# Kernel optimization log

Hardware: AMD Instinct MI355X
Metric: run time of the kernel (lower is better)

## Reference

```python
import jax, jax.numpy as jnp
import numpy as np

ALPHA = 0.2  # tf.nn.leaky_relu default

def leaky(x):
    return jnp.where(x >= 0, x, ALPHA * x)

def segment_softmax(score, seg, num_segments):
    m = jax.ops.segment_max(score, seg, num_segments=num_segments)
    e = jnp.exp(score - m[seg])
    denom = jax.ops.segment_sum(e, seg, num_segments=num_segments)
    return e / denom[seg]

def setup_inputs() -> dict:
    key = jax.random.key(0)
    ks = jax.random.split(key, 8)
    E, NE, NR, D, U = 500000, 100000, 1000, 128, 128
    return {
        "h_index": jax.random.randint(ks[0], (E,), 0, NE),
        "r_index": jax.random.randint(ks[1], (E,), 0, NR),
        "t_index": jax.random.randint(ks[2], (E,), 0, NE),
        "entity_embeddings": jax.random.normal(ks[3], (NE, D), jnp.float32),
        "relation_embeddings": jax.random.normal(ks[4], (NR, D), jnp.float32),
        "W": jax.random.normal(ks[5], (3 * D, U), jnp.float32) * 0.05,
        "a": jax.random.normal(ks[6], (U, 1), jnp.float32) * 0.1,
        "a_b": jnp.zeros((1,), jnp.float32),
        "bias": jnp.zeros((U,), jnp.float32),
    }

def reference(h_index, r_index, t_index, entity_embeddings, relation_embeddings, W, a, a_b, bias):
    num_entities = entity_embeddings.shape[0]
    h = entity_embeddings[h_index]          # [E, D]
    r = relation_embeddings[r_index]        # [E, D]
    t = entity_embeddings[t_index]          # [E, D]
    feats = jnp.concatenate([h, r, t], axis=-1) @ W  # [E, U]
    # att_kernel Dense(1, activation=leaky_relu), then wrapped again in att_activation
    score = leaky(leaky(feats @ a + a_b))[:, 0]      # [E]
    alpha = segment_softmax(score, h_index, num_entities)
    msg = feats * alpha[:, None]                     # gcn_mapper: edge features * weight
    reduced = jax.ops.segment_sum(msg, h_index, num_segments=num_entities)  # [NE, U]
    out = reduced + bias                             # identity_updater returns reduced_msg
    return jax.nn.relu(out)
```

## Files before the change

### kernel.cpp

```cpp
#include <hip/hip_runtime.h>
#include <hip/hip_bf16.h>

#define ALPHA2 0.04f
#define LDA 136

typedef __attribute__((ext_vector_type(8))) short short8;
typedef __attribute__((ext_vector_type(4))) float floatx4;
typedef __attribute__((ext_vector_type(8))) unsigned short ushort8;

__device__ __forceinline__ unsigned short f2bf(float f) {
    unsigned u = __float_as_uint(f);
    unsigned r = (u + 0x7fffu + ((u >> 16) & 1u)) >> 16;
    return (unsigned short)r;
}
__device__ __forceinline__ float bf2f(unsigned short h) {
    return __uint_as_float((unsigned)h << 16);
}


__global__ void k_prep(const float* __restrict__ W, unsigned short* __restrict__ Bfr,
                       int* __restrict__ count, int NE) {
    int idx = blockIdx.x * blockDim.x + threadIdx.x;
    if (idx < 3 * 128 * 128) {
        int kk = idx & 7, n = (idx >> 3) & 127, g = idx >> 10;
        int slice = g >> 4, kc = (g >> 2) & 3, quad = g & 3;
        int k = kc * 32 + quad * 8 + kk;
        Bfr[idx] = f2bf(W[(size_t)(slice * 128 + k) * 128 + n]);
    }
    if (idx < NE) count[idx] = 0;
}

__global__ __launch_bounds__(256, 4) void k_gemm_all(
        const float* __restrict__ ent, const float* __restrict__ rel,
        const unsigned short* __restrict__ Bfr,
        unsigned short* __restrict__ Pb, unsigned short* __restrict__ Qb,
        unsigned short* __restrict__ Rb,
        float* __restrict__ s1, float* __restrict__ s3, float* __restrict__ s2,
        const float* __restrict__ avec, int NE, int NR, int NBent) {
    __shared__ unsigned short Ash[64 * LDA];
    int tid = threadIdx.x;
    int b = blockIdx.x;
    bool isEnt = b < NBent;
    const float* In = isEnt ? ent : rel;
    int nrows = isEnt ? NE : NR;
    int rowbase = (isEnt ? b : b - NBent) * 64;

    #pragma unroll
    for (int it = 0; it < 8; ++it) {
        int id = it * 256 + tid;
        int chunk = id & 31, row = id >> 5;
        int grow = rowbase + row;
        if (grow > nrows - 1) grow = nrows - 1;
        float4 v = *(const float4*)(In + (size_t)grow * 128 + chunk * 4);
        ushort4 u = make_ushort4(f2bf(v.x), f2bf(v.y), f2bf(v.z), f2bf(v.w));
        *(ushort4*)(Ash + row * LDA + chunk * 4) = u;
    }
    __syncthreads();

    int wave = tid >> 6, lane = tid & 63;
    int m16 = lane & 15, quad = lane >> 4;
    int rs = wave * 16;

    float av[8];
    #pragma unroll
    for (int j = 0; j < 8; ++j) av[j] = avec[j * 16 + m16];

    int nphase = isEnt ? 2 : 1;
    for (int ph = 0; ph < nphase; ++ph) {
        int slice; unsigned short* Out; float* svec;
        if (isEnt) { slice = ph ? 2 : 0; Out = ph ? Qb : Pb; svec = ph ? s3 : s1; }
        else       { slice = 1; Out = Rb; svec = s2; }

        floatx4 acc[8];
        #pragma unroll
        for (int j = 0; j < 8; ++j) acc[j] = (floatx4){0.f, 0.f, 0.f, 0.f};

        short8 bf0[8], bf1[8];
        auto loadB = [&](int kc, short8* dst) {
            const unsigned short* bb =
                Bfr + (size_t)((slice * 4 + kc) * 4 + quad) * 1024 + m16 * 8;
            #pragma unroll
            for (int j = 0; j < 8; ++j) dst[j] = *(const short8*)(bb + j * 128);
        };
        auto doMfma = [&](int kc, short8* bf) {
            short8 af = *(const short8*)(Ash + (rs + m16) * LDA + kc * 32 + quad * 8);
            #pragma unroll
            for (int j = 0; j < 8; ++j)
                acc[j] = __builtin_amdgcn_mfma_f32_16x16x32_bf16(af, bf[j], acc[j], 0, 0, 0);
        };
        loadB(0, bf0);
        loadB(1, bf1);
        doMfma(0, bf0);
        loadB(2, bf0);
        doMfma(1, bf1);
        loadB(3, bf1);
        doMfma(2, bf0);
        doMfma(3, bf1);

        #pragma unroll
        for (int reg = 0; reg < 4; ++reg) {
            int row = rowbase + rs + quad * 4 + reg;
            float part = 0.f;
            ushort8 v;
            #pragma unroll
            for (int j = 0; j < 8; ++j) {
                float x = acc[j][reg];
                part = fmaf(x, av[j], part);
                v[j] = f2bf(x);
            }
            #pragma unroll
            for (int off = 1; off < 16; off <<= 1) part += __shfl_xor(part, off);
            if (row < nrows) {
                *(ushort8*)(Out + (size_t)row * 128 + m16 * 8) = v;
                if (m16 == 0) svec[row] = part;
            }
        }
    }
}

__global__ void k_count(const int* __restrict__ h, int* __restrict__ count,
                        int* __restrict__ rank, int E) {
    int e = blockIdx.x * blockDim.x + threadIdx.x;
    if (e < E) rank[e] = atomicAdd(count + h[e], 1);
}

__device__ __forceinline__ int block_incl_scan256(int s, int* sh, int t) {
    sh[t] = s; __syncthreads();
    #pragma unroll
    for (int off = 1; off < 256; off <<= 1) {
        int x = 0;
        if (t >= off) x = sh[t - off];
        __syncthreads();
        sh[t] += x;
        __syncthreads();
    }
    return sh[t];
}

__global__ __launch_bounds__(256) void k_scan_a(const int* __restrict__ count, int NE,
                                                int* __restrict__ bsum) {
    __shared__ int sh[256];
    int b = blockIdx.x, t = threadIdx.x;
    int base = b * 1024 + t * 4, s = 0;
    #pragma unroll
    for (int j = 0; j < 4; ++j) { int i = base + j; if (i < NE) s += count[i]; }
    sh[t] = s; __syncthreads();
    for (int off = 128; off > 0; off >>= 1) {
        if (t < off) sh[t] += sh[t + off];
        __syncthreads();
    }
    if (t == 0) bsum[b] = sh[0];
}

__global__ __launch_bounds__(256) void k_scan_b(int* __restrict__ bsum, int NB) {
    __shared__ int sh[256];
    int t = threadIdx.x;
    int v[4]; int s = 0;
    #pragma unroll
    for (int j = 0; j < 4; ++j) { int i = t * 4 + j; v[j] = (i < NB) ? bsum[i] : 0; s += v[j]; }
    int incl = block_incl_scan256(s, sh, t);
    int excl = incl - s;
    #pragma unroll
    for (int j = 0; j < 4; ++j) {
        int i = t * 4 + j;
        if (i < NB) { int tmp = v[j]; bsum[i] = excl; excl += tmp; }
    }
}

__global__ __launch_bounds__(256) void k_scan_c(const int* __restrict__ count, int NE,
                                                const int* __restrict__ bsum,
                                                int* __restrict__ rowstart, int E) {
    __shared__ int sh[256];
    int b = blockIdx.x, t = threadIdx.x;
    int base = b * 1024 + t * 4;
    int v[4]; int s = 0;
    #pragma unroll
    for (int j = 0; j < 4; ++j) { int i = base + j; v[j] = (i < NE) ? count[i] : 0; s += v[j]; }
    int incl = block_incl_scan256(s, sh, t);
    int excl = bsum[b] + incl - s;
    #pragma unroll
    for (int j = 0; j < 4; ++j) {
        int i = base + j;
        if (i < NE) { rowstart[i] = excl; excl += v[j]; }
    }
    if (b == 0 && t == 0) rowstart[NE] = E;
}

__global__ void k_score_scatter(const int* __restrict__ h, const int* __restrict__ r,
                                const int* __restrict__ t, const float* __restrict__ s1,
                                const float* __restrict__ s2, const float* __restrict__ s3,
                                const float* __restrict__ a_b,
                                const int* __restrict__ rowstart, const int* __restrict__ rank,
                                uint2* __restrict__ rt_s, int E) {
    int e = blockIdx.x * blockDim.x + threadIdx.x;
    if (e >= E) return;
    int hi = h[e], ri = r[e], ti = t[e];
    float x = s1[hi] + s2[ri] + s3[ti] + a_b[0];
    float sc = (x >= 0.f) ? x : ALPHA2 * x;
    float ev = __expf(sc);
    rt_s[rowstart[hi] + rank[e]] = make_uint2(((unsigned)ri << 17) | (unsigned)ti,
                                              __float_as_uint(ev));
}

__global__ __launch_bounds__(256) void k_aggregate(const int* __restrict__ rowstart,
                                                   const uint2* __restrict__ rt_s,
                                                   const unsigned short* __restrict__ Pb,
                                                   const unsigned short* __restrict__ Qb,
                                                   const unsigned short* __restrict__ Rb,
                                                   const float* __restrict__ bias,
                                                   float* __restrict__ out, int NE) {
    int gid = blockIdx.x * blockDim.x + threadIdx.x;
    int n = gid >> 4;
    int sl = gid & 15;
    if (n >= NE) return;
    int start = rowstart[n], end = rowstart[n + 1];
    int c0 = sl * 8;
    float acc[8] = {};
    float evsum = 0.f;
    int i = start;
    for (; i + 4 <= end; i += 4) {
        uint2 m0 = rt_s[i], m1 = rt_s[i + 1], m2 = rt_s[i + 2], m3 = rt_s[i + 3];
        float ev0 = __uint_as_float(m0.y), ev1 = __uint_as_float(m1.y);
        float ev2 = __uint_as_float(m2.y), ev3 = __uint_as_float(m3.y);
        ushort8 q0 = *(const ushort8*)(Qb + (size_t)(m0.x & 0x1FFFFu) * 128 + c0);
        ushort8 rr0 = *(const ushort8*)(Rb + (size_t)(m0.x >> 17) * 128 + c0);
        ushort8 q1 = *(const ushort8*)(Qb + (size_t)(m1.x & 0x1FFFFu) * 128 + c0);
        ushort8 rr1 = *(const ushort8*)(Rb + (size_t)(m1.x >> 17) * 128 + c0);
        ushort8 q2 = *(const ushort8*)(Qb + (size_t)(m2.x & 0x1FFFFu) * 128 + c0);
        ushort8 rr2 = *(const ushort8*)(Rb + (size_t)(m2.x >> 17) * 128 + c0);
        ushort8 q3 = *(const ushort8*)(Qb + (size_t)(m3.x & 0x1FFFFu) * 128 + c0);
        ushort8 rr3 = *(const ushort8*)(Rb + (size_t)(m3.x >> 17) * 128 + c0);
        evsum += (ev0 + ev1) + (ev2 + ev3);
        #pragma unroll
        for (int j = 0; j < 8; ++j) {
            acc[j] = fmaf(ev0, bf2f(q0[j]) + bf2f(rr0[j]), acc[j]);
            acc[j] = fmaf(ev1, bf2f(q1[j]) + bf2f(rr1[j]), acc[j]);
            acc[j] = fmaf(ev2, bf2f(q2[j]) + bf2f(rr2[j]), acc[j]);
            acc[j] = fmaf(ev3, bf2f(q3[j]) + bf2f(rr3[j]), acc[j]);
        }
    }
    for (; i < end; ++i) {
        uint2 m0 = rt_s[i];
        float ev0 = __uint_as_float(m0.y);
        ushort8 q0 = *(const ushort8*)(Qb + (size_t)(m0.x & 0x1FFFFu) * 128 + c0);
        ushort8 rr0 = *(const ushort8*)(Rb + (size_t)(m0.x >> 17) * 128 + c0);
        evsum += ev0;
        #pragma unroll
        for (int j = 0; j < 8; ++j)
            acc[j] = fmaf(ev0, bf2f(q0[j]) + bf2f(rr0[j]), acc[j]);
    }
    float bi[8];
    #pragma unroll
    for (int j = 0; j < 8; ++j) bi[j] = bias[j * 16 + sl];
    float o[8];
    if (end > start) {
        float inv = 1.f / evsum;
        ushort8 pb = *(const ushort8*)(Pb + (size_t)n * 128 + c0);
        #pragma unroll
        for (int j = 0; j < 8; ++j) o[j] = bf2f(pb[j]) + acc[j] * inv + bi[j];
    } else {
        #pragma unroll
        for (int j = 0; j < 8; ++j) o[j] = bi[j];
    }
    #pragma unroll
    for (int j = 0; j < 8; ++j)
        out[(size_t)n * 128 + j * 16 + sl] = fmaxf(o[j], 0.f);
}

static inline size_t align_up(size_t x, size_t a) { return (x + a - 1) / a * a; }

extern "C" void kernel_launch(void* const* d_in, const int* in_sizes, int n_in,
                              void* d_out, int out_size, void* d_ws, size_t ws_size,
                              hipStream_t stream) {
    const int* h_index = (const int*)d_in[0];
    const int* r_index = (const int*)d_in[1];
    const int* t_index = (const int*)d_in[2];
    const float* ent = (const float*)d_in[3];
    const float* rel = (const float*)d_in[4];
    const float* W = (const float*)d_in[5];
    const float* a = (const float*)d_in[6];
    const float* a_b = (const float*)d_in[7];
    const float* bias = (const float*)d_in[8];
    float* out = (float*)d_out;

    int E = in_sizes[0];
    int NE = in_sizes[3] / 128;
    int NR = in_sizes[4] / 128;

    char* p = (char*)d_ws;
    auto alloc = [&](size_t bytes) { char* q = p; p += align_up(bytes, 256); return (void*)q; };
    unsigned short* Pb = (unsigned short*)alloc((size_t)NE * 128 * 2);
    unsigned short* Qb = (unsigned short*)alloc((size_t)NE * 128 * 2);
    unsigned short* Rb = (unsigned short*)alloc((size_t)NR * 128 * 2);
    unsigned short* Bfr = (unsigned short*)alloc((size_t)3 * 128 * 128 * 2);
    float* s1 = (float*)alloc((size_t)NE * 4);
    float* s3 = (float*)alloc((size_t)NE * 4);
    float* s2 = (float*)alloc((size_t)NR * 4);
    int* count = (int*)alloc((size_t)NE * 4);
    int* rowstart = (int*)alloc((size_t)(NE + 1) * 4);
    int* rank = (int*)alloc((size_t)E * 4);
    int NB = (NE + 1023) / 1024;
    int* bsum = (int*)alloc((size_t)NB * 4);
    uint2* rt_s = (uint2*)alloc((size_t)E * 8);
    (void)ws_size; (void)n_in; (void)out_size;

    int nprep = (NE > 3 * 128 * 128) ? NE : 3 * 128 * 128;
    k_prep<<<(nprep + 255) / 256, 256, 0, stream>>>(W, Bfr, count, NE);
    k_count<<<(E + 255) / 256, 256, 0, stream>>>(h_index, count, rank, E);
    int NBent = (NE + 63) / 64, NBrel = (NR + 63) / 64;
    k_gemm_all<<<NBent + NBrel, 256, 0, stream>>>(ent, rel, Bfr, Pb, Qb, Rb,
                                                  s1, s3, s2, a, NE, NR, NBent);
    k_scan_a<<<NB, 256, 0, stream>>>(count, NE, bsum);
    k_scan_b<<<1, 256, 0, stream>>>(bsum, NB);
    k_scan_c<<<NB, 256, 0, stream>>>(count, NE, bsum, rowstart, E);
    k_score_scatter<<<(E + 255) / 256, 256, 0, stream>>>(h_index, r_index, t_index,
                                                         s1, s2, s3, a_b, rowstart,
                                                         rank, rt_s, E);
    k_aggregate<<<(NE * 16 + 255) / 256, 256, 0, stream>>>(rowstart, rt_s, Pb, Qb, Rb,
                                                           bias, out, NE);
}
```

Measured before the change: 207.9 us.

## Async-load fp32 tiles to LDS, fold count into GEMM launch, merge scan passes

The GEMM staging now uses global_load_lds async copies of fp32 rows into a swizzled LDS tile and converts to bf16 at MFMA operand load, rather than converting through registers. The edge count/rank atomic pass runs as extra blocks appended to the GEMM grid, removing one launch. The single-block scan_b is dropped: each scan_c block rescans the block sums itself. The costs are a larger fp32 LDS tile (32KB, which may lower occupancy), repeated bf16 conversion per phase, and redundant bsum scans in every scan_c block.

```diff
diff --git a/kernel.cpp b/kernel.cpp
--- a/kernel.cpp
+++ b/kernel.cpp
@@ -2,7 +2,6 @@
 #include <hip/hip_bf16.h>
 
 #define ALPHA2 0.04f
-#define LDA 136
 
 typedef __attribute__((ext_vector_type(8))) short short8;
 typedef __attribute__((ext_vector_type(4))) float floatx4;
@@ -15,6 +14,12 @@
 }
 __device__ __forceinline__ float bf2f(unsigned short h) {
     return __uint_as_float((unsigned)h << 16);
+}
+
+__device__ __forceinline__ void async_copy16(const float* g, float* lds_base) {
+    __builtin_amdgcn_global_load_lds(
+        (const __attribute__((address_space(1))) unsigned int*)g,
+        (__attribute__((address_space(3))) unsigned int*)lds_base, 16, 0, 0);
 }
 
 
@@ -36,30 +41,42 @@
         unsigned short* __restrict__ Pb, unsigned short* __restrict__ Qb,
         unsigned short* __restrict__ Rb,
         float* __restrict__ s1, float* __restrict__ s3, float* __restrict__ s2,
-        const float* __restrict__ avec, int NE, int NR, int NBent) {
-    __shared__ unsigned short Ash[64 * LDA];
+        const float* __restrict__ avec, int NE, int NR, int NBent, int NBrel,
+        const int* __restrict__ hidx, int* __restrict__ count,
+        int* __restrict__ rank, int E) {
+    __shared__ __align__(16) float Ash[64 * 128];
     int tid = threadIdx.x;
     int b = blockIdx.x;
+    int ngemm = NBent + NBrel;
+
+    if (b >= ngemm) {
+        int e = (b - ngemm) * 256 + tid;
+        if (e < E) rank[e] = atomicAdd(count + hidx[e], 1);
+        return;
+    }
+
     bool isEnt = b < NBent;
     const float* In = isEnt ? ent : rel;
     int nrows = isEnt ? NE : NR;
     int rowbase = (isEnt ? b : b - NBent) * 64;
 
-    #pragma unroll
-    for (int it = 0; it < 8; ++it) {
-        int id = it * 256 + tid;
-        int chunk = id & 31, row = id >> 5;
-        int grow = rowbase + row;
+    int wave = tid >> 6, lane = tid & 63;
+
+    #pragma unroll
+    for (int i = 0; i < 8; ++i) {
+        int r = wave * 16 + i * 2 + (lane >> 5);
+        int grow = rowbase + r;
         if (grow > nrows - 1) grow = nrows - 1;
-        float4 v = *(const float4*)(In + (size_t)grow * 128 + chunk * 4);
-        ushort4 u = make_ushort4(f2bf(v.x), f2bf(v.y), f2bf(v.z), f2bf(v.w));
-        *(ushort4*)(Ash + row * LDA + chunk * 4) = u;
+        int c = (lane & 31) ^ (r & 7);
+        async_copy16(In + (size_t)grow * 128 + c * 4,
+                     Ash + (size_t)(wave * 16 + i * 2) * 128);
     }
     __syncthreads();
 
-    int wave = tid >> 6, lane = tid & 63;
     int m16 = lane & 15, quad = lane >> 4;
     int rs = wave * 16;
+    int R = rs + m16, sw = R & 7;
+    const float4* rowp = (const float4*)(Ash + (size_t)R * 128);
 
     float av[8];
     #pragma unroll
@@ -83,7 +100,14 @@
             for (int j = 0; j < 8; ++j) dst[j] = *(const short8*)(bb + j * 128);
         };
         auto doMfma = [&](int kc, short8* bf) {
-            short8 af = *(const short8*)(Ash + (rs + m16) * LDA + kc * 32 + quad * 8);
+            int c0 = kc * 8 + quad * 2;
+            float4 fa = rowp[c0 ^ sw];
+            float4 fb = rowp[(c0 + 1) ^ sw];
+            short8 af;
+            af[0] = (short)f2bf(fa.x); af[1] = (short)f2bf(fa.y);
+            af[2] = (short)f2bf(fa.z); af[3] = (short)f2bf(fa.w);
+            af[4] = (short)f2bf(fb.x); af[5] = (short)f2bf(fb.y);
+            af[6] = (short)f2bf(fb.z); af[7] = (short)f2bf(fb.w);
             #pragma unroll
             for (int j = 0; j < 8; ++j)
                 acc[j] = __builtin_amdgcn_mfma_f32_16x16x32_bf16(af, bf[j], acc[j], 0, 0, 0);
@@ -118,12 +142,6 @@
     }
 }
 
-__global__ void k_count(const int* __restrict__ h, int* __restrict__ count,
-                        int* __restrict__ rank, int E) {
-    int e = blockIdx.x * blockDim.x + threadIdx.x;
-    if (e < E) rank[e] = atomicAdd(count + h[e], 1);
-}
-
 __device__ __forceinline__ int block_incl_scan256(int s, int* sh, int t) {
     sh[t] = s; __syncthreads();
     #pragma unroll
@@ -152,32 +170,21 @@
     if (t == 0) bsum[b] = sh[0];
 }
 
-__global__ __launch_bounds__(256) void k_scan_b(int* __restrict__ bsum, int NB) {
-    __shared__ int sh[256];
-    int t = threadIdx.x;
-    int v[4]; int s = 0;
-    #pragma unroll
-    for (int j = 0; j < 4; ++j) { int i = t * 4 + j; v[j] = (i < NB) ? bsum[i] : 0; s += v[j]; }
-    int incl = block_incl_scan256(s, sh, t);
-    int excl = incl - s;
-    #pragma unroll
-    for (int j = 0; j < 4; ++j) {
-        int i = t * 4 + j;
-        if (i < NB) { int tmp = v[j]; bsum[i] = excl; excl += tmp; }
-    }
-}
-
 __global__ __launch_bounds__(256) void k_scan_c(const int* __restrict__ count, int NE,
-                                                const int* __restrict__ bsum,
+                                                const int* __restrict__ bsum, int NB,
                                                 int* __restrict__ rowstart, int E) {
     __shared__ int sh[256];
     int b = blockIdx.x, t = threadIdx.x;
+    int sb = (t < NB) ? bsum[t] : 0;
+    (void)block_incl_scan256(sb, sh, t);
+    int base0 = (b == 0) ? 0 : sh[b - 1];
+    __syncthreads();
     int base = b * 1024 + t * 4;
     int v[4]; int s = 0;
     #pragma unroll
     for (int j = 0; j < 4; ++j) { int i = base + j; v[j] = (i < NE) ? count[i] : 0; s += v[j]; }
     int incl = block_incl_scan256(s, sh, t);
-    int excl = bsum[b] + incl - s;
+    int excl = base0 + incl - s;
     #pragma unroll
     for (int j = 0; j < 4; ++j) {
         int i = base + j;
@@ -306,13 +313,13 @@
 
     int nprep = (NE > 3 * 128 * 128) ? NE : 3 * 128 * 128;
     k_prep<<<(nprep + 255) / 256, 256, 0, stream>>>(W, Bfr, count, NE);
-    k_count<<<(E + 255) / 256, 256, 0, stream>>>(h_index, count, rank, E);
     int NBent = (NE + 63) / 64, NBrel = (NR + 63) / 64;
-    k_gemm_all<<<NBent + NBrel, 256, 0, stream>>>(ent, rel, Bfr, Pb, Qb, Rb,
-                                                  s1, s3, s2, a, NE, NR, NBent);
+    int NBcnt = (E + 255) / 256;
+    k_gemm_all<<<NBent + NBrel + NBcnt, 256, 0, stream>>>(
+        ent, rel, Bfr, Pb, Qb, Rb, s1, s3, s2, a, NE, NR, NBent, NBrel,
+        h_index, count, rank, E);
     k_scan_a<<<NB, 256, 0, stream>>>(count, NE, bsum);
-    k_scan_b<<<1, 256, 0, stream>>>(bsum, NB);
-    k_scan_c<<<NB, 256, 0, stream>>>(count, NE, bsum, rowstart, E);
+    k_scan_c<<<NB, 256, 0, stream>>>(count, NE, bsum, NB, rowstart, E);
     k_score_scatter<<<(E + 255) / 256, 256, 0, stream>>>(h_index, r_index, t_index,
                                                          s1, s2, s3, a_b, rowstart,
                                                          rank, rt_s, E);
```

After: 200.3 us. -3.7%, faster.
